# Performance work log

Hardware: AMD Instinct MI355X
Metric: run time of the kernel (lower is better)

The kernel has to match this reference:

```python
import jax, jax.numpy as jnp
import numpy as np

# hyperparameters (from init_kwargs)
GAMMA = 2.0
KEEP_WEIGHT = 1.0
T_TEMP = 0.07
M = 0.5
COS_M = float(np.cos(M))
SIN_M = float(np.sin(M))
THRESHOLD = float(np.cos(np.pi - M))
MM = float(np.sin(np.pi - M) * M)
ALPHA = 0.1
T_BUF0 = 0.0  # registered buffer t initialized to zero
VALID_THRESHOLD = 0.8
EPS = 1e-12  # F.normalize eps


def setup_inputs() -> dict:
    key = jax.random.key(0)
    k1, k2, k3 = jax.random.split(key, 3)
    N, C = 8192, 128
    return {
        "feature1": jax.random.normal(k1, (N, C), jnp.float32),
        "feature2": jax.random.normal(k2, (N, C), jnp.float32),
        "labels": jax.random.randint(k3, (N,), 0, 1024, dtype=jnp.int32),
    }


def reference(feature1, feature2, labels):
    N = feature1.shape[0]
    f1 = feature1 / jnp.maximum(jnp.linalg.norm(feature1, axis=1, keepdims=True), EPS)
    f2 = feature2 / jnp.maximum(jnp.linalg.norm(feature2, axis=1, keepdims=True), EPS)

    # [N, N] similarity, clamped to [-1, 1]
    sim = jnp.clip(jnp.einsum('nc,kc->nk', f1, f2), -1.0, 1.0)

    pos = (labels[:, None] == labels[None, :]).astype(sim.dtype)  # [N, N]
    neg = 1.0 - pos
    pos_mask = pos > 0

    # buffer update t (no_grad in original)
    mean_ts = jax.lax.stop_gradient((sim * pos).sum() / pos.sum())
    t = ALPHA * mean_ts + (1.0 - ALPHA) * T_BUF0
    weight_valid = t > VALID_THRESHOLD

    # curricular margin on positive entries
    sin_theta = jnp.sqrt(1.0 - sim * sim)
    cos_theta_m = sim * COS_M - sin_theta * SIN_M
    final_pos = jnp.where(sim > THRESHOLD, cos_theta_m, sim - MM)
    sim2 = jnp.where(pos_mask, final_pos, sim)

    # per-row mean of (margined) positive similarities
    row_target = (sim2 * pos).sum(axis=1) / pos.sum(axis=1)  # [N]
    hard_mask = sim2 > row_target[:, None]
    sim3 = jnp.where(hard_mask, sim2 * (t + sim2), sim2)
    sim4 = jnp.where(pos_mask, final_pos, sim3)

    logits = jnp.exp(sim4 / T_TEMP)

    # focal-style reweighting (only used when weight_valid)
    diff_pos = (pos - sim * pos) ** GAMMA + KEEP_WEIGHT * pos
    diff_neg = jnp.clip(sim * neg, 0.0, 1.0) ** GAMMA + KEEP_WEIGHT * neg

    logit_pos = jnp.where(weight_valid, (logits * diff_pos).sum(axis=1), (logits * pos).sum(axis=1))
    logit_neg = jnp.where(weight_valid, (logits * diff_neg).sum(axis=1), (logits * neg).sum(axis=1))

    loss = -jnp.log(logit_pos / (logit_neg + logit_pos)).sum() / N
    return loss
```

## Files before the change

### kernel.cpp

```cpp
#include <hip/hip_runtime.h>

#define N_ROWS 8192
#define N_LBL  1024
#define KMAX   64

constexpr float C_COS_M  = (float)0.8775825618903728;
constexpr float C_SIN_M  = (float)0.479425538604203;
constexpr float C_THRESH = (float)-0.8775825618903728;
constexpr float C_MM     = (float)0.2397127693021015;
constexpr float C_ALPHA  = 0.1f;
constexpr float C_VALID  = 0.8f;
constexpr float C_K2E    = (float)(1.0 / (0.07 * 0.6931471805599453));
constexpr float C_LN2    = 0.6931471805599453f;

typedef short s16x8 __attribute__((ext_vector_type(8)));
typedef float f32x4 __attribute__((ext_vector_type(4)));

__device__ __forceinline__ unsigned f2bf(float f) {
    unsigned u = __float_as_uint(f);
    return (u + 0x7fffu + ((u >> 16) & 1u)) >> 16;
}
__device__ __forceinline__ float bflo(unsigned u) { return __uint_as_float(u << 16); }
__device__ __forceinline__ float bfhi(unsigned u) { return __uint_as_float(u & 0xffff0000u); }

__device__ __forceinline__ void gl_lds16(const unsigned* g, void* lds) {
    __builtin_amdgcn_global_load_lds(
        (const __attribute__((address_space(1))) unsigned*)g,
        (__attribute__((address_space(3))) unsigned*)lds, 16, 0, 0);
}

__global__ void k_norm(const float* __restrict__ f1, const float* __restrict__ f2,
                       const int* __restrict__ labels,
                       unsigned* __restrict__ f1n, unsigned* __restrict__ f2n,
                       int* __restrict__ hist, unsigned short* __restrict__ bucket,
                       float* __restrict__ out) {
    if (blockIdx.x == 0 && threadIdx.x == 0) out[0] = 0.f;
    int b = blockIdx.x * 4 + (threadIdx.x >> 6);
    int l = threadIdx.x & 63;
    int row = (b < N_ROWS) ? b : (b - N_ROWS);
    const float* src = (b < N_ROWS) ? f1 : f2;
    unsigned* dst = (b < N_ROWS) ? f1n : f2n;
    float2 v = ((const float2*)(src + row * 128))[l];
    float ss = v.x * v.x + v.y * v.y;
    #pragma unroll
    for (int k = 1; k < 64; k <<= 1) ss += __shfl_xor(ss, k);
    float inv = 1.0f / fmaxf(sqrtf(ss), 1e-12f);
    dst[row * 64 + l] = f2bf(v.x * inv) | (f2bf(v.y * inv) << 16);
    if (b < N_ROWS && l == 0) {
        int lab = labels[row];
        int p = atomicAdd(&hist[lab], 1);
        if (p < KMAX) bucket[lab * KMAX + p] = (unsigned short)row;
    }
}

__global__ __launch_bounds__(64) void k_passA(const unsigned* __restrict__ f1n,
                                              const unsigned* __restrict__ f2n,
                                              const int* __restrict__ labels,
                                              const int* __restrict__ hist,
                                              const unsigned short* __restrict__ bucket,
                                              float* __restrict__ rt,
                                              float* __restrict__ row_sim,
                                              int* __restrict__ rowcnt,
                                              float* __restrict__ simlist) {
    int i = blockIdx.x, lane = threadIdx.x;
    int g = lane >> 4, sl = lane & 15;
    uint4 a = ((const uint4*)(f1n + i * 64))[sl];
    float a0 = bflo(a.x), a1 = bfhi(a.x), a2 = bflo(a.y), a3 = bfhi(a.y);
    float a4 = bflo(a.z), a5 = bfhi(a.z), a6 = bflo(a.w), a7 = bfhi(a.w);
    int lab = labels[i];
    int cnt = hist[lab];
    int cntc = cnt < KMAX ? cnt : KMAX;
    float rs_sim = 0.f, rs_fp = 0.f;
    for (int e0 = 0; e0 < cntc; e0 += 4) {
        int e = e0 + g;
        bool val = e < cntc;
        int j = bucket[lab * KMAX + (val ? e : 0)];
        uint4 b = ((const uint4*)(f2n + j * 64))[sl];
        float p = a0 * bflo(b.x) + a1 * bfhi(b.x) + a2 * bflo(b.y) + a3 * bfhi(b.y)
                + a4 * bflo(b.z) + a5 * bfhi(b.z) + a6 * bflo(b.w) + a7 * bfhi(b.w);
        p += __shfl_xor(p, 1);
        p += __shfl_xor(p, 2);
        p += __shfl_xor(p, 4);
        p += __shfl_xor(p, 8);
        float s = fminf(1.f, fmaxf(-1.f, p));
        float ctm = s * C_COS_M - sqrtf(fmaxf(0.f, 1.f - s * s)) * C_SIN_M;
        float fpv = (s > C_THRESH) ? ctm : (s - C_MM);
        if (val) {
            rs_sim += s;
            rs_fp += fpv;
            if (sl == 0) simlist[i * KMAX + e] = s;
        }
    }
    rs_sim += __shfl_xor(rs_sim, 16); rs_sim += __shfl_xor(rs_sim, 32);
    rs_fp  += __shfl_xor(rs_fp, 16);  rs_fp  += __shfl_xor(rs_fp, 32);
    if (lane == 0) {
        rt[i] = rs_fp / (float)cnt;
        row_sim[i] = rs_sim;
        rowcnt[i] = cnt;
    }
}

__global__ void k_finalize(const float* __restrict__ row_sim, const int* __restrict__ hist,
                           float* __restrict__ tw) {
    int t = threadIdx.x;
    float ssum = 0.f, scnt = 0.f;
    if (t < N_LBL) { float h = (float)hist[t]; scnt = h * h; }
    #pragma unroll
    for (int p = 0; p < 8; ++p) ssum += row_sim[p * 1024 + t];
    #pragma unroll
    for (int k = 1; k < 64; k <<= 1) {
        ssum += __shfl_xor(ssum, k);
        scnt += __shfl_xor(scnt, k);
    }
    __shared__ float sa[16], sb[16];
    if ((t & 63) == 0) { sa[t >> 6] = ssum; sb[t >> 6] = scnt; }
    __syncthreads();
    if (t == 0) {
        float s1 = 0.f, s2 = 0.f;
        #pragma unroll
        for (int w = 0; w < 16; ++w) { s1 += sa[w]; s2 += sb[w]; }
        tw[0] = C_ALPHA * s1 / s2;
    }
}

template <bool WV>
__device__ __forceinline__ void epi_accum(const f32x4 (&acc)[4][2], const float (&rtv)[4][4],
                                          float (&lnp)[4][4], float tval) {
    #pragma unroll
    for (int mt = 0; mt < 4; ++mt)
        #pragma unroll
        for (int nt = 0; nt < 2; ++nt)
            #pragma unroll
            for (int r = 0; r < 4; ++r) {
                float s = acc[mt][nt][r];
                float u = C_K2E * s;
                float m = tval + s;
                float arg = (s > rtv[mt][r]) ? u * m : u;
                float e = __builtin_amdgcn_exp2f(arg);
                if (WV) { float cz = fmaxf(s, 0.f); e *= cz * cz + 1.f; }
                lnp[mt][r] += e;
            }
}

__global__ __launch_bounds__(512, 4) void k_passB(const unsigned* __restrict__ f1n,
                                                  const unsigned* __restrict__ f2n,
                                                  const float* __restrict__ rt,
                                                  const float* __restrict__ tw,
                                                  float* __restrict__ lnacc2) {
    __shared__ __align__(16) unsigned char ldsA[32768];
    __shared__ __align__(16) unsigned char ldsB[32768];
    const int tid = threadIdx.x;
    const int wave = tid >> 6, lane = tid & 63;
    const int wr = wave >> 2, wc = wave & 3;
    const int quad = lane >> 4, l15 = lane & 15;
    const int rowbase = blockIdx.x * 128;
    const float tval = tw[0];
    const bool wv = (tval > C_VALID);

    const int srow = tid >> 4;
    const int sq   = (tid & 15) ^ (srow & 15);
    const int goff = srow * 64 + sq * 4;
    const int loff = wave * 1024;

    {
        const unsigned* gA = f1n + rowbase * 64 + goff;
        const unsigned* gB = f2n + (blockIdx.y * 1024) * 64 + goff;
        #pragma unroll
        for (int it = 0; it < 4; ++it) {
            gl_lds16(gA + it * 2048, ldsA + loff + it * 8192);
            gl_lds16(gB + it * 2048, ldsB + loff + it * 8192);
        }
    }

    float rtv[4][4];
    #pragma unroll
    for (int mt = 0; mt < 4; ++mt)
        #pragma unroll
        for (int r = 0; r < 4; ++r)
            rtv[mt][r] = rt[rowbase + wr * 64 + mt * 16 + quad * 4 + r];

    __syncthreads();

    float lnp[4][4] = {};
    #pragma unroll 1
    for (int ctile = 0; ctile < 8; ++ctile) {
        f32x4 zero = {0.f, 0.f, 0.f, 0.f};
        f32x4 acc[4][2];
        #pragma unroll
        for (int mt = 0; mt < 4; ++mt)
            #pragma unroll
            for (int nt = 0; nt < 2; ++nt) acc[mt][nt] = zero;

        #pragma unroll
        for (int ks = 0; ks < 4; ++ks) {
            s16x8 af[4], bfr[2];
            #pragma unroll
            for (int mt = 0; mt < 4; ++mt) {
                int row = wr * 64 + mt * 16 + l15, q = ks * 4 + quad;
                af[mt] = *((const s16x8*)(ldsA + row * 256 + ((q ^ (row & 15)) << 4)));
            }
            #pragma unroll
            for (int nt = 0; nt < 2; ++nt) {
                int row = wc * 32 + nt * 16 + l15, q = ks * 4 + quad;
                bfr[nt] = *((const s16x8*)(ldsB + row * 256 + ((q ^ (row & 15)) << 4)));
            }
            #pragma unroll
            for (int mt = 0; mt < 4; ++mt)
                #pragma unroll
                for (int nt = 0; nt < 2; ++nt)
                    acc[mt][nt] = __builtin_amdgcn_mfma_f32_16x16x32_bf16(af[mt], bfr[nt],
                                                                          acc[mt][nt], 0, 0, 0);
        }

        __syncthreads();
        if (ctile < 7) {
            const unsigned* gB = f2n + (blockIdx.y * 1024 + (ctile + 1) * 128) * 64 + goff;
            #pragma unroll
            for (int it = 0; it < 4; ++it)
                gl_lds16(gB + it * 2048, ldsB + loff + it * 8192);
        }

        if (wv) epi_accum<true>(acc, rtv, lnp, tval);
        else    epi_accum<false>(acc, rtv, lnp, tval);

        if (ctile < 7) __syncthreads();
    }

    const int slice = blockIdx.y * 4 + wc;
    #pragma unroll
    for (int mt = 0; mt < 4; ++mt)
        #pragma unroll
        for (int r = 0; r < 4; ++r) {
            float v = lnp[mt][r];
            v += __shfl_xor(v, 1);
            v += __shfl_xor(v, 2);
            v += __shfl_xor(v, 4);
            v += __shfl_xor(v, 8);
            if (l15 == 0)
                lnacc2[slice * N_ROWS + rowbase + wr * 64 + mt * 16 + quad * 4 + r] = v;
        }
}

__global__ void k_lossC(const float* __restrict__ simlist, const int* __restrict__ rowcnt,
                        const float* __restrict__ rt, const float* __restrict__ tw,
                        const float* __restrict__ lnacc2, float* __restrict__ out) {
    int t = threadIdx.x;
    int sub = t >> 3, sl = t & 7;
    int i = blockIdx.x * 32 + sub;
    int cnt = rowcnt[i];
    if (cnt > KMAX) cnt = KMAX;
    float tval = tw[0];
    bool wv = (tval > C_VALID);
    float rti = rt[i];
    float lp = 0.f, den = 0.f;
    for (int e = sl; e < cnt; e += 8) {
        float s = simlist[i * KMAX + e];
        float sh = (s > rti) ? s * (tval + s) : s;
        float en = __builtin_amdgcn_exp2f(C_K2E * sh);
        float ctm = s * C_COS_M - sqrtf(fmaxf(0.f, 1.f - s * s)) * C_SIN_M;
        float fp = (s > C_THRESH) ? ctm : (s - C_MM);
        float ep = __builtin_amdgcn_exp2f(C_K2E * fp);
        if (wv) {
            float cz = fmaxf(s, 0.f);
            en *= cz * cz + 1.f;
            float d = 1.f - s;
            ep *= d * d + 1.f;
        }
        den -= en;
        lp += ep;
    }
    float lnsum = 0.f;
    #pragma unroll
    for (int p = 0; p < 4; ++p) lnsum += lnacc2[(sl + p * 8) * N_ROWS + i];
    #pragma unroll
    for (int k = 1; k < 8; k <<= 1) {
        den += __shfl_xor(den, k);
        lp += __shfl_xor(lp, k);
        lnsum += __shfl_xor(lnsum, k);
    }
    float ln = lnsum + den;
    float rl = (__builtin_amdgcn_logf(lp + ln) - __builtin_amdgcn_logf(lp)) * C_LN2;
    rl += __shfl_xor(rl, 8);
    rl += __shfl_xor(rl, 16);
    rl += __shfl_xor(rl, 32);
    __shared__ float sa[4];
    if ((t & 63) == 0) sa[t >> 6] = rl;
    __syncthreads();
    if (t == 0)
        atomicAdd(out, (sa[0] + sa[1] + sa[2] + sa[3]) * (1.0f / (float)N_ROWS));
}

extern "C" void kernel_launch(void* const* d_in, const int* in_sizes, int n_in,
                              void* d_out, int out_size, void* d_ws, size_t ws_size,
                              hipStream_t stream) {
    (void)in_sizes; (void)n_in; (void)out_size; (void)ws_size;
    const float* f1 = (const float*)d_in[0];
    const float* f2 = (const float*)d_in[1];
    const int* labels = (const int*)d_in[2];
    float* out = (float*)d_out;
    char* ws = (char*)d_ws;

    unsigned* f1n          = (unsigned*)(ws + 0);
    unsigned* f2n          = (unsigned*)(ws + 2097152);
    float* simlist         = (float*)(ws + 4194304);
    float* rt              = (float*)(ws + 6291456);
    float* row_sim         = (float*)(ws + 6324224);
    int* rowcnt            = (int*)(ws + 6356992);
    float* lnacc2          = (float*)(ws + 6389760);
    unsigned short* bucket = (unsigned short*)(ws + 7438336);
    float* tw              = (float*)(ws + 7569408);
    int* hist              = (int*)(ws + 7569472);

    hipMemsetAsync(hist, 0, 4096, stream);

    k_norm<<<dim3(4096), dim3(256), 0, stream>>>(f1, f2, labels, f1n, f2n, hist, bucket, out);
    k_passA<<<dim3(N_ROWS), dim3(64), 0, stream>>>(f1n, f2n, labels, hist, bucket,
                                                   rt, row_sim, rowcnt, simlist);
    k_finalize<<<dim3(1), dim3(1024), 0, stream>>>(row_sim, hist, tw);
    k_passB<<<dim3(64, 8), dim3(512), 0, stream>>>(f1n, f2n, rt, tw, lnacc2);
    k_lossC<<<dim3(256), dim3(256), 0, stream>>>(simlist, rowcnt, rt, tw, lnacc2, out);
}
```

Measured before the change: 127.3 us.

## Keep A fragments in registers and stream B directly from global memory

k_passB now runs 256-thread blocks of 4 waves. Each wave loads its 64-row A tile into registers once, then streams B fragments straight from global memory with a two-deep register double buffer, instead of staging B tiles through LDS behind block-wide barriers. This removes the LDS round-trip for B and the per-tile __syncthreads. The cost is uncoalesced 16-byte per-lane global loads, higher register pressure from holding 16 A fragments, and fewer waves per block. The per-row partial slices drop from 32 to 16, so the lnacc2 reduction in k_lossC and the workspace offsets are adjusted to match.

Result: faster. 117.9 us (-7.4%).

```diff
diff --git a/kernel.cpp b/kernel.cpp
--- a/kernel.cpp
+++ b/kernel.cpp
@@ -123,53 +123,28 @@
     }
 }
 
-template <bool WV>
-__device__ __forceinline__ void epi_accum(const f32x4 (&acc)[4][2], const float (&rtv)[4][4],
-                                          float (&lnp)[4][4], float tval) {
-    #pragma unroll
-    for (int mt = 0; mt < 4; ++mt)
-        #pragma unroll
-        for (int nt = 0; nt < 2; ++nt)
-            #pragma unroll
-            for (int r = 0; r < 4; ++r) {
-                float s = acc[mt][nt][r];
-                float u = C_K2E * s;
-                float m = tval + s;
-                float arg = (s > rtv[mt][r]) ? u * m : u;
-                float e = __builtin_amdgcn_exp2f(arg);
-                if (WV) { float cz = fmaxf(s, 0.f); e *= cz * cz + 1.f; }
-                lnp[mt][r] += e;
-            }
-}
-
-__global__ __launch_bounds__(512, 4) void k_passB(const unsigned* __restrict__ f1n,
+__global__ __launch_bounds__(256, 3) void k_passB(const unsigned* __restrict__ f1n,
                                                   const unsigned* __restrict__ f2n,
                                                   const float* __restrict__ rt,
                                                   const float* __restrict__ tw,
                                                   float* __restrict__ lnacc2) {
     __shared__ __align__(16) unsigned char ldsA[32768];
-    __shared__ __align__(16) unsigned char ldsB[32768];
     const int tid = threadIdx.x;
     const int wave = tid >> 6, lane = tid & 63;
-    const int wr = wave >> 2, wc = wave & 3;
+    const int wr = wave >> 1, wc = wave & 1;
     const int quad = lane >> 4, l15 = lane & 15;
     const int rowbase = blockIdx.x * 128;
     const float tval = tw[0];
     const bool wv = (tval > C_VALID);
 
-    const int srow = tid >> 4;
-    const int sq   = (tid & 15) ^ (srow & 15);
-    const int goff = srow * 64 + sq * 4;
-    const int loff = wave * 1024;
-
     {
-        const unsigned* gA = f1n + rowbase * 64 + goff;
-        const unsigned* gB = f2n + (blockIdx.y * 1024) * 64 + goff;
-        #pragma unroll
-        for (int it = 0; it < 4; ++it) {
-            gl_lds16(gA + it * 2048, ldsA + loff + it * 8192);
-            gl_lds16(gB + it * 2048, ldsB + loff + it * 8192);
-        }
+        const int srow = tid >> 4;
+        const int sq   = (tid & 15) ^ (srow & 15);
+        const unsigned* gA = f1n + rowbase * 64 + srow * 64 + sq * 4;
+        const int loff = wave * 1024;
+        #pragma unroll
+        for (int it = 0; it < 8; ++it)
+            gl_lds16(gA + it * 1024, ldsA + loff + it * 4096);
     }
 
     float rtv[4][4];
@@ -181,52 +156,60 @@
 
     __syncthreads();
 
+    s16x8 af[4][4];
+    #pragma unroll
+    for (int mt = 0; mt < 4; ++mt)
+        #pragma unroll
+        for (int ks = 0; ks < 4; ++ks) {
+            int row = wr * 64 + mt * 16 + l15, q = ks * 4 + quad;
+            af[mt][ks] = *((const s16x8*)(ldsA + row * 256 + ((q ^ (row & 15)) << 4)));
+        }
+
+    const unsigned* bb = f2n + (blockIdx.y * 1024 + wc * 512 + l15) * 64 + quad * 4;
+
     float lnp[4][4] = {};
-    #pragma unroll 1
-    for (int ctile = 0; ctile < 8; ++ctile) {
-        f32x4 zero = {0.f, 0.f, 0.f, 0.f};
-        f32x4 acc[4][2];
+
+    auto loadB = [&](s16x8* b, int ct) {
+        const unsigned* p = bb + ct * 1024;
+        #pragma unroll
+        for (int ks = 0; ks < 4; ++ks)
+            b[ks] = *((const s16x8*)(p + ks * 16));
+    };
+    auto tile = [&](const s16x8* b) {
+        f32x4 acc[4];
+        #pragma unroll
+        for (int mt = 0; mt < 4; ++mt) acc[mt] = (f32x4){0.f, 0.f, 0.f, 0.f};
+        #pragma unroll
+        for (int ks = 0; ks < 4; ++ks)
+            #pragma unroll
+            for (int mt = 0; mt < 4; ++mt)
+                acc[mt] = __builtin_amdgcn_mfma_f32_16x16x32_bf16(af[mt][ks], b[ks],
+                                                                  acc[mt], 0, 0, 0);
         #pragma unroll
         for (int mt = 0; mt < 4; ++mt)
             #pragma unroll
-            for (int nt = 0; nt < 2; ++nt) acc[mt][nt] = zero;
-
-        #pragma unroll
-        for (int ks = 0; ks < 4; ++ks) {
-            s16x8 af[4], bfr[2];
-            #pragma unroll
-            for (int mt = 0; mt < 4; ++mt) {
-                int row = wr * 64 + mt * 16 + l15, q = ks * 4 + quad;
-                af[mt] = *((const s16x8*)(ldsA + row * 256 + ((q ^ (row & 15)) << 4)));
+            for (int r = 0; r < 4; ++r) {
+                float s = acc[mt][r];
+                float u = C_K2E * s;
+                float m = tval + s;
+                float arg = (s > rtv[mt][r]) ? u * m : u;
+                float e = __builtin_amdgcn_exp2f(arg);
+                if (wv) { float cz = fmaxf(s, 0.f); e = e * (cz * cz + 1.f); }
+                lnp[mt][r] += e;
             }
-            #pragma unroll
-            for (int nt = 0; nt < 2; ++nt) {
-                int row = wc * 32 + nt * 16 + l15, q = ks * 4 + quad;
-                bfr[nt] = *((const s16x8*)(ldsB + row * 256 + ((q ^ (row & 15)) << 4)));
-            }
-            #pragma unroll
-            for (int mt = 0; mt < 4; ++mt)
-                #pragma unroll
-                for (int nt = 0; nt < 2; ++nt)
-                    acc[mt][nt] = __builtin_amdgcn_mfma_f32_16x16x32_bf16(af[mt], bfr[nt],
-                                                                          acc[mt][nt], 0, 0, 0);
-        }
-
-        __syncthreads();
-        if (ctile < 7) {
-            const unsigned* gB = f2n + (blockIdx.y * 1024 + (ctile + 1) * 128) * 64 + goff;
-            #pragma unroll
-            for (int it = 0; it < 4; ++it)
-                gl_lds16(gB + it * 2048, ldsB + loff + it * 8192);
-        }
-
-        if (wv) epi_accum<true>(acc, rtv, lnp, tval);
-        else    epi_accum<false>(acc, rtv, lnp, tval);
-
-        if (ctile < 7) __syncthreads();
-    }
-
-    const int slice = blockIdx.y * 4 + wc;
+    };
+
+    s16x8 b0[4], b1[4];
+    loadB(b0, 0);
+    #pragma unroll 1
+    for (int ct = 0; ct < 32; ct += 2) {
+        loadB(b1, ct + 1);
+        tile(b0);
+        if (ct + 2 < 32) loadB(b0, ct + 2);
+        tile(b1);
+    }
+
+    const int slice = blockIdx.y * 2 + wc;
     #pragma unroll
     for (int mt = 0; mt < 4; ++mt)
         #pragma unroll
@@ -271,7 +254,7 @@
     }
     float lnsum = 0.f;
     #pragma unroll
-    for (int p = 0; p < 4; ++p) lnsum += lnacc2[(sl + p * 8) * N_ROWS + i];
+    for (int p = 0; p < 2; ++p) lnsum += lnacc2[(sl + p * 8) * N_ROWS + i];
     #pragma unroll
     for (int k = 1; k < 8; k <<= 1) {
         den += __shfl_xor(den, k);
@@ -307,9 +290,9 @@
     float* row_sim         = (float*)(ws + 6324224);
     int* rowcnt            = (int*)(ws + 6356992);
     float* lnacc2          = (float*)(ws + 6389760);
-    unsigned short* bucket = (unsigned short*)(ws + 7438336);
-    float* tw              = (float*)(ws + 7569408);
-    int* hist              = (int*)(ws + 7569472);
+    unsigned short* bucket = (unsigned short*)(ws + 6914048);
+    float* tw              = (float*)(ws + 7045120);
+    int* hist              = (int*)(ws + 7045184);
 
     hipMemsetAsync(hist, 0, 4096, stream);
 
@@ -317,6 +300,6 @@
     k_passA<<<dim3(N_ROWS), dim3(64), 0, stream>>>(f1n, f2n, labels, hist, bucket,
                                                    rt, row_sim, rowcnt, simlist);
     k_finalize<<<dim3(1), dim3(1024), 0, stream>>>(row_sim, hist, tw);
-    k_passB<<<dim3(64, 8), dim3(512), 0, stream>>>(f1n, f2n, rt, tw, lnacc2);
+    k_passB<<<dim3(64, 8), dim3(256), 0, stream>>>(f1n, f2n, rt, tw, lnacc2);
     k_lossC<<<dim3(256), dim3(256), 0, stream>>>(simlist, rowcnt, rt, tw, lnacc2, out);
 }
```
